# Kernel tuning notes

Hardware: AMD Instinct MI355X
Metric: run time of the kernel (lower is better)

## Reference

```python
import jax, jax.numpy as jnp
import numpy as np

NUM_GROUPS = 32
EPS = 1e-5


def group_norm(x, w, b):
    # x: [B, C, H, W]
    B, C, H, W = x.shape
    g = x.reshape(B, NUM_GROUPS, C // NUM_GROUPS, H, W)
    mu = g.mean(axis=(2, 3, 4), keepdims=True)
    var = g.var(axis=(2, 3, 4), keepdims=True)
    g = (g - mu) * jax.lax.rsqrt(var + EPS)
    x = g.reshape(B, C, H, W)
    return x * w[None, :, None, None] + b[None, :, None, None]


def conv1x1(x, w, b):
    # 1x1 conv == channel matmul; x: [B, C, H, W], w: [O, C], b: [O]
    return jnp.einsum('bchw,oc->bohw', x, w) + b[None, :, None, None]


def setup_inputs() -> dict:
    key = jax.random.key(0)
    ks = jax.random.split(key, 11)
    C = 512
    B, H, W = 4, 64, 64
    s = 1.0 / np.sqrt(C)
    return {
        'x': jax.random.normal(ks[0], (B, C, H, W), jnp.float32),
        'gn_w': jax.random.uniform(ks[1], (C,), jnp.float32, 0.5, 1.5),
        'gn_b': jax.random.normal(ks[2], (C,), jnp.float32) * 0.1,
        'wq': jax.random.normal(ks[3], (C, C), jnp.float32) * s,
        'bq': jax.random.normal(ks[4], (C,), jnp.float32) * 0.01,
        'wk': jax.random.normal(ks[5], (C, C), jnp.float32) * s,
        'bk': jax.random.normal(ks[6], (C,), jnp.float32) * 0.01,
        'wv': jax.random.normal(ks[7], (C, C), jnp.float32) * s,
        'bv': jax.random.normal(ks[8], (C,), jnp.float32) * 0.01,
        'wo': jax.random.normal(ks[9], (C, C), jnp.float32) * s,
        'bo': jax.random.normal(ks[10], (C,), jnp.float32) * 0.01,
    }


def reference(x, gn_w, gn_b, wq, bq, wk, bk, wv, bv, wo, bo):
    B, C, H, W = x.shape
    h_ = group_norm(x, gn_w, gn_b)
    q = conv1x1(h_, wq, bq).reshape(B, C, H * W)   # [B, C, HW]
    k = conv1x1(h_, wk, bk).reshape(B, C, H * W)
    v = conv1x1(h_, wv, bv).reshape(B, C, H * W)
    # scores: q^T k, scaled by C^-0.5; softmax over keys
    scores = jnp.einsum('bci,bcj->bij', q, k) * (C ** -0.5)  # [B, HW, HW]
    attn = jax.nn.softmax(scores, axis=-1)
    # h_[b,c,i] = sum_j v[b,c,j] * attn[b,i,j]
    h_ = jnp.einsum('bcj,bij->bci', v, attn).reshape(B, C, H, W)
    return x + conv1x1(h_, wo, bo)
```

## Files before the change

### kernel.cpp

```cpp
#include <hip/hip_runtime.h>
#include <hip/hip_bf16.h>

typedef __attribute__((ext_vector_type(8))) __bf16 bf16x8;
typedef __attribute__((ext_vector_type(4))) float f32x4;

__device__ __forceinline__ unsigned short f2bf(float f) {
  union { float f; unsigned u; } v; v.f = f;
  unsigned r = v.u + 0x7fffu + ((v.u >> 16) & 1u);
  return (unsigned short)(r >> 16);
}

__device__ __forceinline__ void gload_lds16(const void* g, void* s) {
  __builtin_amdgcn_global_load_lds(
      (const __attribute__((address_space(1))) void*)g,
      (__attribute__((address_space(3))) void*)s, 16, 0, 0);
}

__global__ __launch_bounds__(256) void convert_w(
    const float* __restrict__ wq, const float* __restrict__ wk,
    const float* __restrict__ wv, const float* __restrict__ wo,
    unsigned short* __restrict__ dst) {
  const int m = blockIdx.x >> 10;
  const float* src = (m == 0) ? wq : (m == 1) ? wk : (m == 2) ? wv : wo;
  const int idx = ((blockIdx.x & 1023) << 8) | threadIdx.x;
  dst[m * 262144 + idx] = f2bf(src[idx]);
}

__global__ __launch_bounds__(256) void zero_k(float* __restrict__ p, int n) {
  const int i = blockIdx.x * 256 + threadIdx.x;
  if (i < n) p[i] = 0.f;
}

__global__ __launch_bounds__(256) void gn_stats(
    const float* __restrict__ x, float2* __restrict__ partials) {
  const int bg = blockIdx.x >> 2, part = blockIdx.x & 3;
  const float* xg = x + (size_t)bg * 65536 + part * 1024;
  const int t = threadIdx.x;
  float s = 0.f, ss = 0.f;
#pragma unroll
  for (int r = 0; r < 16; ++r) {
    const float4 v = *(const float4*)(xg + (size_t)r * 4096 + t * 4);
    s += v.x + v.y + v.z + v.w;
    ss += v.x * v.x + v.y * v.y + v.z * v.z + v.w * v.w;
  }
#pragma unroll
  for (int m = 32; m; m >>= 1) { s += __shfl_xor(s, m); ss += __shfl_xor(ss, m); }
  __shared__ float red[8];
  const int wave = t >> 6, lane = t & 63;
  if (lane == 0) { red[wave] = s; red[wave + 4] = ss; }
  __syncthreads();
  if (t == 0) {
    float2 p;
    p.x = red[0] + red[1] + red[2] + red[3];
    p.y = red[4] + red[5] + red[6] + red[7];
    partials[blockIdx.x] = p;
  }
}

__global__ __launch_bounds__(256) void gn_apply(
    const float* __restrict__ x, const float2* __restrict__ partials,
    const float* __restrict__ gw, const float* __restrict__ gb,
    unsigned short* __restrict__ h_t) {
  const int bg = blockIdx.x >> 3, cc = blockIdx.x & 7;
  const int b = bg >> 5, g = bg & 31;
  const int t = threadIdx.x;
  __shared__ float chs[32];
  __shared__ unsigned short tile[16][520];
  if (t < 16) {
    const float2 p0 = partials[bg * 4 + 0], p1 = partials[bg * 4 + 1];
    const float2 p2 = partials[bg * 4 + 2], p3 = partials[bg * 4 + 3];
    const float S = p0.x + p1.x + p2.x + p3.x;
    const float SS = p0.y + p1.y + p2.y + p3.y;
    const float mu = S * (1.f / 65536.f);
    const float rstd = rsqrtf(SS * (1.f / 65536.f) - mu * mu + 1e-5f);
    const float sc = gw[g * 16 + t] * rstd;
    chs[t] = sc;
    chs[16 + t] = gb[g * 16 + t] - mu * sc;
  }
  __syncthreads();
  const float* xg = x + (size_t)bg * 65536 + cc * 512;
#pragma unroll
  for (int rr = 0; rr < 8; ++rr) {
    const int r = rr * 2 + (t >> 7), i = (t & 127) * 4;
    const float4 v = *(const float4*)(xg + (size_t)r * 4096 + i);
    const float sc = chs[r], sh = chs[16 + r];
    ushort4 o;
    o.x = f2bf(v.x * sc + sh); o.y = f2bf(v.y * sc + sh);
    o.z = f2bf(v.z * sc + sh); o.w = f2bf(v.w * sc + sh);
    *(ushort4*)&tile[r][i] = o;
  }
  __syncthreads();
  unsigned short* outp = h_t + ((size_t)b * 4096 + cc * 512) * 512 + g * 16;
#pragma unroll
  for (int rep = 0; rep < 4; ++rep) {
    const int task = rep * 256 + t;
    const int nl = task >> 1, half = (task & 1) * 8;
    ushort4 o0, o1;
    o0.x = tile[half + 0][nl]; o0.y = tile[half + 1][nl];
    o0.z = tile[half + 2][nl]; o0.w = tile[half + 3][nl];
    o1.x = tile[half + 4][nl]; o1.y = tile[half + 5][nl];
    o1.z = tile[half + 6][nl]; o1.w = tile[half + 7][nl];
    *(ushort4*)(outp + (size_t)nl * 512 + half) = o0;
    *(ushort4*)(outp + (size_t)nl * 512 + half + 4) = o1;
  }
}

__global__ __launch_bounds__(256) void reduce4_k(
    const float* __restrict__ part, const float* __restrict__ l,
    unsigned short* __restrict__ dst) {
  const size_t i = ((size_t)blockIdx.x * 256 + threadIdx.x) * 4;
  f32x4 s0 = *(const f32x4*)(part + i);
  f32x4 s1 = *(const f32x4*)(part + 2097152 + i);
  f32x4 s2 = *(const f32x4*)(part + 4194304 + i);
  f32x4 s3 = *(const f32x4*)(part + 6291456 + i);
  f32x4 s = (s0 + s1) + (s2 + s3);
  const float inv = 1.f / l[i >> 9];
  ushort4 o;
  o.x = f2bf(s[0] * inv); o.y = f2bf(s[1] * inv);
  o.z = f2bf(s[2] * inv); o.w = f2bf(s[3] * inv);
  *(ushort4*)(dst + i) = o;
}

__global__ __launch_bounds__(512, 4) void gemm_s256(
    const unsigned short* __restrict__ A, const unsigned short* __restrict__ Bt,
    unsigned short* __restrict__ Out, float* __restrict__ lsum) {
  __shared__ __align__(16) char smem[73728];
  const int tid = threadIdx.x;
  const int wave = tid >> 6, lane = tid & 63;
  const int l15 = lane & 15, l4 = lane >> 4;
  const int wm = wave >> 1, wn = wave & 1;

  const int bz = blockIdx.z;
  A += (size_t)bz * 2097152;
  Bt += (size_t)bz * 2097152;
  Out += (size_t)bz * 16777216;
  lsum += (size_t)bz * 4096;

  const int id = blockIdx.y * 32 + blockIdx.x;
  const int xcd = id & 7, j = id >> 3;
  const int by = ((xcd >> 1) << 2) + (j >> 4);
  const int bx = ((xcd & 1) << 4) + (j & 15);
  const int row0 = by << 8, col0 = bx << 7;

  const int ar = tid >> 2;
  const int akc = (tid & 3) ^ ((tid >> 4) & 3);

  auto stage = [&](int kt, int bi) {
    const int kb = kt << 5;
    char* base = smem + bi * 24576;
    const unsigned short* gA = A + (size_t)(row0 + ar) * 512 + kb + akc * 8;
    const unsigned short* gB = Bt + (size_t)(col0 + ar) * 512 + kb + akc * 8;
    gload_lds16(gA, base + wave * 1024);
    gload_lds16(gA + (size_t)128 * 512, base + 8192 + wave * 1024);
    gload_lds16(gB, base + 16384 + wave * 1024);
  };

  f32x4 acc[4][4];
#pragma unroll
  for (int r = 0; r < 4; ++r)
#pragma unroll
    for (int c = 0; c < 4; ++c) acc[r][c] = (f32x4)0.f;

  const int xsw = (l4 ^ (l15 >> 2)) << 4;

  auto compute = [&](int bi) {
    const char* pa = smem + bi * 24576 + (wm * 64 + l15) * 64 + xsw;
    const char* pb = smem + bi * 24576 + 16384 + (wn * 64 + l15) * 64 + xsw;
    bf16x8 af[4], bfr[4];
#pragma unroll
    for (int r = 0; r < 4; ++r) af[r] = *(const bf16x8*)(pa + r * 1024);
#pragma unroll
    for (int c = 0; c < 4; ++c) bfr[c] = *(const bf16x8*)(pb + c * 1024);
#pragma unroll
    for (int r = 0; r < 4; ++r)
#pragma unroll
      for (int c = 0; c < 4; ++c)
        acc[r][c] = __builtin_amdgcn_mfma_f32_16x16x32_bf16(af[r], bfr[c], acc[r][c], 0, 0, 0);
  };

  stage(0, 0);
  stage(1, 1);
  int bi = 0;
  for (int kt = 0; kt < 15; ++kt) {
    asm volatile("s_waitcnt vmcnt(3)" ::: "memory");
    __builtin_amdgcn_s_barrier();
    __builtin_amdgcn_sched_barrier(0);
    if (kt + 2 < 16) stage(kt + 2, (kt + 2) % 3);
    compute(bi);
    bi = (bi == 2) ? 0 : bi + 1;
  }
  asm volatile("s_waitcnt vmcnt(0)" ::: "memory");
  __builtin_amdgcn_s_barrier();
  __builtin_amdgcn_sched_barrier(0);
  compute(bi);

  __syncthreads();
  unsigned short* tile = (unsigned short*)smem;
#pragma unroll
  for (int p = 0; p < 2; ++p) {
    if ((wm >> 1) == p) {
#pragma unroll
      for (int c = 0; c < 4; ++c) {
        const int coll = wn * 64 + c * 16 + l15;
#pragma unroll
        for (int r = 0; r < 4; ++r) {
          const int rowl = (wm & 1) * 64 + r * 16 + l4 * 4;
#pragma unroll
          for (int j = 0; j < 4; ++j)
            tile[(rowl + j) * 136 + coll] = f2bf(__expf(acc[r][c][j]));
        }
      }
    }
    __syncthreads();
#pragma unroll
    for (int it = 0; it < 4; ++it) {
      const int idx = it * 512 + tid;
      const int rw = idx >> 4, ch = (idx & 15) * 8;
      const uint4 vv = *(const uint4*)&tile[rw * 136 + ch];
      *(uint4*)(Out + (size_t)(row0 + p * 128 + rw) * 4096 + col0 + ch) = vv;
      const unsigned* uu = (const unsigned*)&vv;
      float s = 0.f;
#pragma unroll
      for (int q = 0; q < 4; ++q) {
        union { unsigned u; float f; } w;
        w.u = uu[q] << 16; s += w.f;
        w.u = uu[q] & 0xffff0000u; s += w.f;
      }
      s += __shfl_xor(s, 1); s += __shfl_xor(s, 2);
      s += __shfl_xor(s, 4); s += __shfl_xor(s, 8);
      if ((lane & 15) == 0) atomicAdd(&lsum[row0 + p * 128 + rw], s);
    }
    __syncthreads();
  }
}

__global__ __launch_bounds__(512, 2) void gemm_s_ps(
    const unsigned short* __restrict__ A, const unsigned short* __restrict__ Bt,
    unsigned short* __restrict__ Out, float* __restrict__ lsum) {
  __shared__ __align__(16) char smem[147456];
  const int tid = threadIdx.x;
  const int wave = tid >> 6, lane = tid & 63;
  const int l15 = lane & 15, l4 = lane >> 4;
  const int wm = wave >> 1, wn = wave & 1;

  const int bz = blockIdx.z;
  A += (size_t)bz * 2097152;
  Bt += (size_t)bz * 2097152;
  Out += (size_t)bz * 16777216;
  lsum += (size_t)bz * 4096;

  const int id = blockIdx.y * 32 + blockIdx.x;
  const int xcd = id & 7, j = id >> 3;
  const int by = ((xcd >> 1) << 2) + (j >> 4);
  const int bx = ((xcd & 1) << 4) + (j & 15);
  const int row0 = by << 8, col0 = bx << 7;

  const int sr = tid >> 3;
  const int sc8 = (tid & 7) ^ (sr & 7);
  const unsigned short* gA = A + (size_t)(row0 + sr) * 512 + sc8 * 8;
  const unsigned short* gB = Bt + (size_t)(col0 + sr) * 512 + sc8 * 8;

  auto stA = [&](int kt, int bi, int p) {
    gload_lds16(gA + (size_t)(p << 6) * 512 + (kt << 6),
                smem + bi * 49152 + p * 8192 + wave * 1024);
  };
  auto stB = [&](int kt, int bi, int p) {
    gload_lds16(gB + (size_t)(p << 6) * 512 + (kt << 6),
                smem + bi * 49152 + 32768 + p * 8192 + wave * 1024);
  };

  f32x4 acc[4][4];
#pragma unroll
  for (int r = 0; r < 4; ++r)
#pragma unroll
    for (int c = 0; c < 4; ++c) acc[r][c] = (f32x4)0.f;

  const int sw0 = (l4 ^ (l15 & 7)) << 4;
  const int sw1 = ((4 + l4) ^ (l15 & 7)) << 4;
  const int arow = (wm * 64 + l15) << 7;
  const int brow = (wn * 64 + l15) << 7;

  bf16x8 bfr[4][2];

  stA(0, 0, 0); stA(0, 0, 1); stA(0, 0, 2); stA(0, 0, 3);
  stB(0, 0, 0); stB(0, 0, 1);
  stA(1, 1, 0); stA(1, 1, 1); stA(1, 1, 2); stA(1, 1, 3);
  stB(1, 1, 0); stB(1, 1, 1);
  asm volatile("s_waitcnt vmcnt(6)" ::: "memory");
  __builtin_amdgcn_s_barrier();
  __builtin_amdgcn_sched_barrier(0);

  int bi = 0;
#pragma unroll 1
  for (int kt = 0; kt < 8; ++kt) {
    const char* bufA = smem + bi * 49152;
    const char* bufB = bufA + 32768;
    const int pb = (bi + 2) % 3;
    const bool pre = (kt + 2 < 8);
    bf16x8 a0, a1;
    a0 = *(const bf16x8*)(bufA + arow + sw0);
    a1 = *(const bf16x8*)(bufA + arow + sw1);
#pragma unroll
    for (int c = 0; c < 4; ++c) {
      bfr[c][0] = *(const bf16x8*)(bufB + brow + c * 2048 + sw0);
      bfr[c][1] = *(const bf16x8*)(bufB + brow + c * 2048 + sw1);
    }
    if (pre) { stA(kt + 2, pb, 0); stA(kt + 2, pb, 1); }
    __builtin_amdgcn_s_barrier();
    asm volatile("s_waitcnt lgkmcnt(0)" ::: "memory");
    __builtin_amdgcn_sched_barrier(0);
    __builtin_amdgcn_s_setprio(1);
#pragma unroll
    for (int c = 0; c < 4; ++c) {
      acc[0][c] = __builtin_amdgcn_mfma_f32_16x16x32_bf16(a0, bfr[c][0], acc[0][c], 0, 0, 0);
      acc[0][c] = __builtin_amdgcn_mfma_f32_16x16x32_bf16(a1, bfr[c][1], acc[0][c], 0, 0, 0);
    }
    __builtin_amdgcn_s_setprio(0);
    __builtin_amdgcn_s_barrier();
    a0 = *(const bf16x8*)(bufA + arow + 2048 + sw0);
    a1 = *(const bf16x8*)(bufA + arow + 2048 + sw1);
    if (pre) { stA(kt + 2, pb, 2); stA(kt + 2, pb, 3); }
    __builtin_amdgcn_s_barrier();
    asm volatile("s_waitcnt lgkmcnt(0)" ::: "memory");
    __builtin_amdgcn_sched_barrier(0);
    __builtin_amdgcn_s_setprio(1);
#pragma unroll
    for (int c = 0; c < 4; ++c) {
      acc[1][c] = __builtin_amdgcn_mfma_f32_16x16x32_bf16(a0, bfr[c][0], acc[1][c], 0, 0, 0);
      acc[1][c] = __builtin_amdgcn_mfma_f32_16x16x32_bf16(a1, bfr[c][1], acc[1][c], 0, 0, 0);
    }
    __builtin_amdgcn_s_setprio(0);
    __builtin_amdgcn_s_barrier();
    a0 = *(const bf16x8*)(bufA + arow + 4096 + sw0);
    a1 = *(const bf16x8*)(bufA + arow + 4096 + sw1);
    if (pre) { stB(kt + 2, pb, 0); stB(kt + 2, pb, 1); }
    __builtin_amdgcn_s_barrier();
    asm volatile("s_waitcnt lgkmcnt(0)" ::: "memory");
    __builtin_amdgcn_sched_barrier(0);
    __builtin_amdgcn_s_setprio(1);
#pragma unroll
    for (int c = 0; c < 4; ++c) {
      acc[2][c] = __builtin_amdgcn_mfma_f32_16x16x32_bf16(a0, bfr[c][0], acc[2][c], 0, 0, 0);
      acc[2][c] = __builtin_amdgcn_mfma_f32_16x16x32_bf16(a1, bfr[c][1], acc[2][c], 0, 0, 0);
    }
    __builtin_amdgcn_s_setprio(0);
    __builtin_amdgcn_s_barrier();
    a0 = *(const bf16x8*)(bufA + arow + 6144 + sw0);
    a1 = *(const bf16x8*)(bufA + arow + 6144 + sw1);
    __builtin_amdgcn_s_barrier();
    asm volatile("s_waitcnt lgkmcnt(0)" ::: "memory");
    __builtin_amdgcn_sched_barrier(0);
    __builtin_amdgcn_s_setprio(1);
#pragma unroll
    for (int c = 0; c < 4; ++c) {
      acc[3][c] = __builtin_amdgcn_mfma_f32_16x16x32_bf16(a0, bfr[c][0], acc[3][c], 0, 0, 0);
      acc[3][c] = __builtin_amdgcn_mfma_f32_16x16x32_bf16(a1, bfr[c][1], acc[3][c], 0, 0, 0);
    }
    __builtin_amdgcn_s_setprio(0);
    if (pre) asm volatile("s_waitcnt vmcnt(6)" ::: "memory");
    else     asm volatile("s_waitcnt vmcnt(0)" ::: "memory");
    __builtin_amdgcn_s_barrier();
    __builtin_amdgcn_sched_barrier(0);
    bi = (bi == 2) ? 0 : bi + 1;
  }

  __syncthreads();
  unsigned short* tile = (unsigned short*)smem;
#pragma unroll
  for (int c = 0; c < 4; ++c) {
    const int coll = wn * 64 + c * 16 + l15;
#pragma unroll
    for (int r = 0; r < 4; ++r) {
      const int rowl = wm * 64 + r * 16 + l4 * 4;
#pragma unroll
      for (int j = 0; j < 4; ++j)
        tile[(rowl + j) * 136 + coll] = f2bf(__expf(acc[r][c][j]));
    }
  }
  __syncthreads();
#pragma unroll
  for (int it = 0; it < 8; ++it) {
    const int idx = it * 512 + tid;
    const int rw = idx >> 4, ch = (idx & 15) * 8;
    const uint4 vv = *(const uint4*)&tile[rw * 136 + ch];
    *(uint4*)(Out + (size_t)(row0 + rw) * 4096 + col0 + ch) = vv;
    const unsigned* uu = (const unsigned*)&vv;
    float s = 0.f;
#pragma unroll
    for (int q = 0; q < 4; ++q) {
      union { unsigned u; float f; } w;
      w.u = uu[q] << 16; s += w.f;
      w.u = uu[q] & 0xffff0000u; s += w.f;
    }
    s += __shfl_xor(s, 1); s += __shfl_xor(s, 2);
    s += __shfl_xor(s, 4); s += __shfl_xor(s, 8);
    if ((lane & 15) == 0) atomicAdd(&lsum[row0 + rw], s);
  }
}

__global__ __launch_bounds__(512, 2) void gemm_pv(
    const unsigned short* __restrict__ P, const unsigned short* __restrict__ Vt,
    unsigned short* __restrict__ Out, const float* __restrict__ lrow) {
  __shared__ __align__(16) char smem[147456];
  const int tid = threadIdx.x;
  const int wave = tid >> 6, lane = tid & 63;
  const int l15 = lane & 15, l4 = lane >> 4;
  const int wm = wave >> 1, wn = wave & 1;

  const int L = blockIdx.x + ((blockIdx.y + (blockIdx.z << 4)) << 2);
  const int xcd = L & 7, j = L >> 3;
  const int panel = xcd * 8 + (j >> 2);
  const int bx = j & 3, by = panel & 15, bz = panel >> 4;
  const int row0 = by << 8, col0 = bx << 7;
  P += (size_t)bz * 16777216;
  Vt += (size_t)bz * 2097152;
  Out += (size_t)bz * 2097152;
  lrow += bz * 4096;

  const int sr = tid >> 3;
  const int sc8 = (tid & 7) ^ (sr & 7);
  const unsigned short* gA = P + (size_t)(row0 + sr) * 4096 + sc8 * 8;
  const unsigned short* gB = Vt + (size_t)(col0 + sr) * 4096 + sc8 * 8;

  auto stA = [&](int kt, int bi, int p) {
    gload_lds16(gA + (size_t)(p << 6) * 4096 + (kt << 6),
                smem + bi * 49152 + p * 8192 + wave * 1024);
  };
  auto stB = [&](int kt, int bi, int p) {
    gload_lds16(gB + (size_t)(p << 6) * 4096 + (kt << 6),
                smem + bi * 49152 + 32768 + p * 8192 + wave * 1024);
  };

  f32x4 acc[4][4];
#pragma unroll
  for (int r = 0; r < 4; ++r)
#pragma unroll
    for (int c = 0; c < 4; ++c) acc[r][c] = (f32x4)0.f;

  const int sw0 = (l4 ^ (l15 & 7)) << 4;
  const int sw1 = ((4 + l4) ^ (l15 & 7)) << 4;
  const int arow = (wm * 64 + l15) << 7;
  const int brow = (wn * 64 + l15) << 7;

  bf16x8 bfr[4][2];

  stA(0, 0, 0); stA(0, 0, 1); stA(0, 0, 2); stA(0, 0, 3);
  stB(0, 0, 0); stB(0, 0, 1);
  stA(1, 1, 0); stA(1, 1, 1); stA(1, 1, 2); stA(1, 1, 3);
  stB(1, 1, 0); stB(1, 1, 1);
  asm volatile("s_waitcnt vmcnt(6)" ::: "memory");
  __builtin_amdgcn_s_barrier();
  __builtin_amdgcn_sched_barrier(0);

  int bi = 0;
#pragma unroll 1
  for (int kt = 0; kt < 64; ++kt) {
    const char* bufA = smem + bi * 49152;
    const char* bufB = bufA + 32768;
    const int pb = (bi + 2) % 3;
    const bool pre = (kt + 2 < 64);
    bf16x8 a0, a1;
    a0 = *(const bf16x8*)(bufA + arow + sw0);
    a1 = *(const bf16x8*)(bufA + arow + sw1);
#pragma unroll
    for (int c = 0; c < 4; ++c) {
      bfr[c][0] = *(const bf16x8*)(bufB + brow + c * 2048 + sw0);
      bfr[c][1] = *(const bf16x8*)(bufB + brow + c * 2048 + sw1);
    }
    if (pre) { stA(kt + 2, pb, 0); stA(kt + 2, pb, 1); }
    __builtin_amdgcn_s_barrier();
    asm volatile("s_waitcnt lgkmcnt(0)" ::: "memory");
    __builtin_amdgcn_sched_barrier(0);
    __builtin_amdgcn_s_setprio(1);
#pragma unroll
    for (int c = 0; c < 4; ++c) {
      acc[0][c] = __builtin_amdgcn_mfma_f32_16x16x32_bf16(a0, bfr[c][0], acc[0][c], 0, 0, 0);
      acc[0][c] = __builtin_amdgcn_mfma_f32_16x16x32_bf16(a1, bfr[c][1], acc[0][c], 0, 0, 0);
    }
    __builtin_amdgcn_s_setprio(0);
    __builtin_amdgcn_s_barrier();
    a0 = *(const bf16x8*)(bufA + arow + 2048 + sw0);
    a1 = *(const bf16x8*)(bufA + arow + 2048 + sw1);
    if (pre) { stA(kt + 2, pb, 2); stA(kt + 2, pb, 3); }
    __builtin_amdgcn_s_barrier();
    asm volatile("s_waitcnt lgkmcnt(0)" ::: "memory");
    __builtin_amdgcn_sched_barrier(0);
    __builtin_amdgcn_s_setprio(1);
#pragma unroll
    for (int c = 0; c < 4; ++c) {
      acc[1][c] = __builtin_amdgcn_mfma_f32_16x16x32_bf16(a0, bfr[c][0], acc[1][c], 0, 0, 0);
      acc[1][c] = __builtin_amdgcn_mfma_f32_16x16x32_bf16(a1, bfr[c][1], acc[1][c], 0, 0, 0);
    }
    __builtin_amdgcn_s_setprio(0);
    __builtin_amdgcn_s_barrier();
    a0 = *(const bf16x8*)(bufA + arow + 4096 + sw0);
    a1 = *(const bf16x8*)(bufA + arow + 4096 + sw1);
    if (pre) { stB(kt + 2, pb, 0); stB(kt + 2, pb, 1); }
    __builtin_amdgcn_s_barrier();
    asm volatile("s_waitcnt lgkmcnt(0)" ::: "memory");
    __builtin_amdgcn_sched_barrier(0);
    __builtin_amdgcn_s_setprio(1);
#pragma unroll
    for (int c = 0; c < 4; ++c) {
      acc[2][c] = __builtin_amdgcn_mfma_f32_16x16x32_bf16(a0, bfr[c][0], acc[2][c], 0, 0, 0);
      acc[2][c] = __builtin_amdgcn_mfma_f32_16x16x32_bf16(a1, bfr[c][1], acc[2][c], 0, 0, 0);
    }
    __builtin_amdgcn_s_setprio(0);
    __builtin_amdgcn_s_barrier();
    a0 = *(const bf16x8*)(bufA + arow + 6144 + sw0);
    a1 = *(const bf16x8*)(bufA + arow + 6144 + sw1);
    __builtin_amdgcn_s_barrier();
    asm volatile("s_waitcnt lgkmcnt(0)" ::: "memory");
    __builtin_amdgcn_sched_barrier(0);
    __builtin_amdgcn_s_setprio(1);
#pragma unroll
    for (int c = 0; c < 4; ++c) {
      acc[3][c] = __builtin_amdgcn_mfma_f32_16x16x32_bf16(a0, bfr[c][0], acc[3][c], 0, 0, 0);
      acc[3][c] = __builtin_amdgcn_mfma_f32_16x16x32_bf16(a1, bfr[c][1], acc[3][c], 0, 0, 0);
    }
    __builtin_amdgcn_s_setprio(0);
    if (pre) asm volatile("s_waitcnt vmcnt(6)" ::: "memory");
    else     asm volatile("s_waitcnt vmcnt(0)" ::: "memory");
    __builtin_amdgcn_s_barrier();
    __builtin_amdgcn_sched_barrier(0);
    bi = (bi == 2) ? 0 : bi + 1;
  }

  __syncthreads();
  unsigned short* tile = (unsigned short*)smem;
#pragma unroll
  for (int c = 0; c < 4; ++c) {
    const int coll = wn * 64 + c * 16 + l15;
#pragma unroll
    for (int r = 0; r < 4; ++r) {
      const int rowl = wm * 64 + r * 16 + l4 * 4;
#pragma unroll
      for (int j = 0; j < 4; ++j) {
        const float v = acc[r][c][j] * (1.0f / lrow[row0 + rowl + j]);
        tile[(rowl + j) * 136 + coll] = f2bf(v);
      }
    }
  }
  __syncthreads();
#pragma unroll
  for (int it = 0; it < 8; ++it) {
    const int idx = it * 512 + tid;
    const int rw = idx >> 4, ch = (idx & 15) * 8;
    const uint4 vv = *(const uint4*)&tile[rw * 136 + ch];
    *(uint4*)(Out + (size_t)(row0 + rw) * 512 + col0 + ch) = vv;
  }
}

template <bool OUT_BF16, int BIAS_MODE, bool RESID, bool TRANS_OUT, int SWZ,
          bool COAL>
__global__ __launch_bounds__(256) void gemm_bt(
    const unsigned short* __restrict__ A, long long sA, int lda,
    const unsigned short* __restrict__ Bt, long long sB, int ldb,
    void* __restrict__ OutV, long long sO, int ldo,
    const float* __restrict__ bias,
    const float* __restrict__ resid, long long sR,
    int K, float scale) {
  __shared__ __align__(16) char smem[49152];
  const int tid = threadIdx.x;
  const int wave = tid >> 6, lane = tid & 63;
  const int l15 = lane & 15, l4 = lane >> 4;
  const int wm = wave >> 1, wn = wave & 1;

  int bx = blockIdx.x, by = blockIdx.y, bz = blockIdx.z;
  if constexpr (SWZ == 1) {
    const int id = by * 32 + bx;
    const int xcd = id & 7, j = id >> 3;
    by = ((xcd >> 1) << 3) + (j >> 4);
    bx = ((xcd & 1) << 4) + (j & 15);
  } else if constexpr (SWZ == 2) {
    const int L = bx + ((by + (bz << 5)) << 2);
    const int xcd = L & 7, j = L >> 3;
    const int pair = xcd * 16 + (j >> 2);
    bx = j & 3;
    by = pair & 31;
    bz = pair >> 5;
  }
  const int row0 = by << 7, col0 = bx << 7;
  A += (size_t)bz * sA;
  Bt += (size_t)bz * sB;
  if (RESID) resid += (size_t)bz * sR;
  if constexpr (BIAS_MODE == 3) bias += (size_t)bz * sR;
  char* outB = (char*)OutV + (size_t)bz * sO * (OUT_BF16 ? 2 : 4);

  const int ar = tid >> 2;
  const int akc = (tid & 3) ^ ((tid >> 4) & 3);

  auto stage = [&](int kt, int bi) {
    const int kb = kt << 5;
    char* sAl = smem + bi * 16384 + wave * 1024;
    char* sBl = sAl + 8192;
    const unsigned short* gA = A + (size_t)(row0 + ar) * lda + kb + akc * 8;
    const unsigned short* gB = Bt + (size_t)(col0 + ar) * ldb + kb + akc * 8;
    gload_lds16(gA, sAl);
    gload_lds16(gB, sBl);
    gload_lds16(gA + (size_t)64 * lda, sAl + 4096);
    gload_lds16(gB + (size_t)64 * ldb, sBl + 4096);
  };

  f32x4 acc[4][4];
#pragma unroll
  for (int r = 0; r < 4; ++r)
#pragma unroll
    for (int c = 0; c < 4; ++c) acc[r][c] = (f32x4)0.f;

  const int nk = K >> 5;
  const int xsw = (l4 ^ (l15 >> 2)) << 4;

  auto compute = [&](int bi) {
    const char* pa = smem + bi * 16384 + (wm * 64 + l15) * 64 + xsw;
    const char* pb = smem + bi * 16384 + 8192 + (wn * 64 + l15) * 64 + xsw;
    bf16x8 af[4], bfr[4];
#pragma unroll
    for (int r = 0; r < 4; ++r) af[r] = *(const bf16x8*)(pa + r * 1024);
#pragma unroll
    for (int c = 0; c < 4; ++c) bfr[c] = *(const bf16x8*)(pb + c * 1024);
#pragma unroll
    for (int r = 0; r < 4; ++r)
#pragma unroll
      for (int c = 0; c < 4; ++c)
        acc[r][c] = __builtin_amdgcn_mfma_f32_16x16x32_bf16(af[r], bfr[c], acc[r][c], 0, 0, 0);
  };

  stage(0, 0);
  stage(1, 1);
  int bi = 0;
  for (int kt = 0; kt < nk - 1; ++kt) {
    asm volatile("s_waitcnt vmcnt(4)" ::: "memory");
    __builtin_amdgcn_s_barrier();
    __builtin_amdgcn_sched_barrier(0);
    if (kt + 2 < nk) stage(kt + 2, (kt + 2) % 3);
    compute(bi);
    bi = (bi == 2) ? 0 : bi + 1;
  }
  asm volatile("s_waitcnt vmcnt(0)" ::: "memory");
  __builtin_amdgcn_s_barrier();
  __builtin_amdgcn_sched_barrier(0);
  compute(bi);

  if constexpr (COAL && !TRANS_OUT) {
    __syncthreads();
    if constexpr (OUT_BF16) {
      unsigned short* tile = (unsigned short*)smem;
#pragma unroll
      for (int c = 0; c < 4; ++c) {
        const int coll = wn * 64 + c * 16 + l15;
        float badd = 0.f;
        if constexpr (BIAS_MODE == 1) badd = bias[col0 + coll];
#pragma unroll
        for (int r = 0; r < 4; ++r) {
          const int rowl = wm * 64 + r * 16 + l4 * 4;
#pragma unroll
          for (int j = 0; j < 4; ++j) {
            float v;
            if constexpr (BIAS_MODE == 3)
              v = acc[r][c][j] * (1.0f / bias[row0 + rowl + j]);
            else
              v = (acc[r][c][j] + badd) * scale;
            tile[(rowl + j) * 136 + coll] = f2bf(v);
          }
        }
      }
      __syncthreads();
      unsigned short* outp = (unsigned short*)outB;
#pragma unroll
      for (int it = 0; it < 8; ++it) {
        const int idx = it * 256 + tid;
        const int rw = idx >> 4, ch = (idx & 15) * 8;
        const uint4 vv = *(const uint4*)&tile[rw * 136 + ch];
        *(uint4*)(outp + (size_t)(row0 + rw) * ldo + col0 + ch) = vv;
      }
    } else {
      float* tile = (float*)smem;
#pragma unroll
      for (int p = 0; p < 2; ++p) {
        if (wm == p) {
#pragma unroll
          for (int c = 0; c < 4; ++c) {
            const int coll = wn * 64 + c * 16 + l15;
            float badd = 0.f;
            if constexpr (BIAS_MODE == 1) badd = bias[col0 + coll];
#pragma unroll
            for (int r = 0; r < 4; ++r) {
              const int rowl = r * 16 + l4 * 4;
#pragma unroll
              for (int j = 0; j < 4; ++j) {
                float v = acc[r][c][j] + badd;
                if constexpr (BIAS_MODE == 2) v += bias[row0 + p * 64 + rowl + j];
                tile[(rowl + j) * 132 + coll] = v * scale;
              }
            }
          }
        }
        __syncthreads();
        float* outp = (float*)outB;
#pragma unroll
        for (int it = 0; it < 8; ++it) {
          const int idx = it * 256 + tid;
          const int rw = idx >> 5, ch = (idx & 31) * 4;
          const int rowg = row0 + p * 64 + rw;
          f32x4 v = *(const f32x4*)&tile[rw * 132 + ch];
          if constexpr (RESID) {
            const float* rp = resid + (size_t)rowg * ldo + col0 + ch;
            v[0] += rp[0]; v[1] += rp[1]; v[2] += rp[2]; v[3] += rp[3];
          }
          *(f32x4*)(outp + (size_t)rowg * ldo + col0 + ch) = v;
        }
        __syncthreads();
      }
    }
  } else if constexpr (!TRANS_OUT) {
#pragma unroll
    for (int c = 0; c < 4; ++c) {
      const int colg = col0 + wn * 64 + c * 16 + l15;
      float badd = 0.f;
      if constexpr (BIAS_MODE == 1) badd = bias[colg];
#pragma unroll
      for (int r = 0; r < 4; ++r) {
        const int rowg = row0 + wm * 64 + r * 16 + l4 * 4;
#pragma unroll
        for (int j = 0; j < 4; ++j) {
          float v = acc[r][c][j] + badd;
          if constexpr (BIAS_MODE == 2) v += bias[rowg + j];
          v *= scale;
          if constexpr (RESID) v += resid[(size_t)(rowg + j) * ldo + colg];
          if constexpr (OUT_BF16)
            ((unsigned short*)outB)[(size_t)(rowg + j) * ldo + colg] = f2bf(v);
          else
            ((float*)outB)[(size_t)(rowg + j) * ldo + colg] = v;
        }
      }
    }
  } else {
    __syncthreads();
    unsigned short* tile = (unsigned short*)smem;
#pragma unroll
    for (int c = 0; c < 4; ++c) {
      const int coll = wn * 64 + c * 16 + l15;
      float badd = 0.f;
      if constexpr (BIAS_MODE == 1) badd = bias[col0 + coll];
#pragma unroll
      for (int r = 0; r < 4; ++r) {
        const int rowl = wm * 64 + r * 16 + l4 * 4;
#pragma unroll
        for (int j = 0; j < 4; ++j)
          tile[(rowl + j) * 132 + coll] = f2bf((acc[r][c][j] + badd) * scale);
      }
    }
    __syncthreads();
    unsigned short* outp = (unsigned short*)outB;
#pragma unroll 8
    for (int it = 0; it < 64; ++it) {
      const int idx = it * 256 + tid;
      const int cl = idx >> 7, il = idx & 127;
      outp[(size_t)(col0 + cl) * ldo + row0 + il] = tile[il * 132 + cl];
    }
  }
}

extern "C" void kernel_launch(void* const* d_in, const int* in_sizes, int n_in,
                              void* d_out, int out_size, void* d_ws, size_t ws_size,
                              hipStream_t stream) {
  const float* x   = (const float*)d_in[0];
  const float* gnw = (const float*)d_in[1];
  const float* gnb = (const float*)d_in[2];
  const float* wq  = (const float*)d_in[3];
  const float* bq  = (const float*)d_in[4];
  const float* wk  = (const float*)d_in[5];
  const float* bk  = (const float*)d_in[6];
  const float* wv  = (const float*)d_in[7];
  const float* bv  = (const float*)d_in[8];
  const float* wo  = (const float*)d_in[9];
  const float* bo  = (const float*)d_in[10];
  float* out = (float*)d_out;
  char* ws = (char*)d_ws;

  const size_t MB = 1u << 20;
  float2*         gnp  = (float2*)ws;
  float*          lrow = (float*)(ws + 64 * 1024);
  unsigned short* wbf  = (unsigned short*)(ws + 1 * MB);
  unsigned short* h_t  = (unsigned short*)(ws + 3 * MB);
  unsigned short* q_t  = (unsigned short*)(ws + 19 * MB);
  unsigned short* k_t  = (unsigned short*)(ws + 35 * MB);
  unsigned short* v_ct = (unsigned short*)(ws + 51 * MB);
  unsigned short* h2_t = (unsigned short*)(ws + 67 * MB);
  unsigned short* Pbuf = (unsigned short*)(ws + 83 * MB);
  float*          part = (float*)(ws + 115 * MB);

  const long long BS = 2097152;
  const long long PBS = 16777216;
  const float qscale = 0.044194173824159216f;
  const bool batched = ws_size >= 212 * MB;

  convert_w<<<dim3(4096), dim3(256), 0, stream>>>(wq, wk, wv, wo, wbf);
  gn_stats<<<dim3(512), dim3(256), 0, stream>>>(x, gnp);
  gn_apply<<<dim3(1024), dim3(256), 0, stream>>>(x, gnp, gnw, gnb, h_t);

  gemm_bt<true, 1, false, false, 0, true><<<dim3(4, 32, 4), 256, 0, stream>>>(
      h_t, BS, 512, wbf + 0, 0, 512, q_t, BS, 512, bq, nullptr, 0, 512, qscale);
  gemm_bt<true, 1, false, false, 0, true><<<dim3(4, 32, 4), 256, 0, stream>>>(
      h_t, BS, 512, wbf + 262144, 0, 512, k_t, BS, 512, bk, nullptr, 0, 512, 1.0f);
  gemm_bt<true, 1, false, true, 0, false><<<dim3(4, 32, 4), 256, 0, stream>>>(
      h_t, BS, 512, wbf + 524288, 0, 512, v_ct, BS, 4096, bv, nullptr, 0, 512, 1.0f);

  if (batched) {
    zero_k<<<dim3(64), dim3(256), 0, stream>>>(lrow, 16384);
    gemm_s_ps<<<dim3(32, 16, 4), dim3(512), 0, stream>>>(q_t, k_t, Pbuf, lrow);
    gemm_pv<<<dim3(4, 16, 4), dim3(512), 0, stream>>>(Pbuf, v_ct, h2_t, lrow);
  } else {
    for (int b = 0; b < 4; ++b) {
      zero_k<<<dim3(16), dim3(256), 0, stream>>>(lrow, 4096);
      gemm_s256<<<dim3(32, 16, 1), dim3(512), 0, stream>>>(
          q_t + (size_t)b * BS, k_t + (size_t)b * BS, Pbuf, lrow);
      gemm_bt<false, 0, false, false, 0, true><<<dim3(4, 32, 4), 256, 0, stream>>>(
          Pbuf, 1024, 4096, v_ct + (size_t)b * BS, 1024, 4096,
          part, 2097152, 512, nullptr, nullptr, 0, 1024, 1.0f);
      reduce4_k<<<dim3(2048), dim3(256), 0, stream>>>(part, lrow, h2_t + (size_t)b * BS);
    }
  }

  gemm_bt<false, 2, true, false, 0, true><<<dim3(32, 4, 4), 256, 0, stream>>>(
      wbf + 786432, 0, 512, h2_t, BS, 512, out, BS, 4096, bo, x, BS, 512, 1.0f);
}
```

Baseline: 295.9 us.

## Make score GEMM persistent, streaming row tiles through continuous K pipeline

Replaces the 2048-block score/exp kernel with a 256-block persistent kernel. Each block keeps one 128-column K tile and walks 8 row tiles of Q through a single 64-step triple-buffered pipeline. Prefetch of the next tile therefore overlaps the exp/bf16 store and row-sum epilogue of the previous tile. The epilogue now runs in two halves through a shared-memory buffer that is still in the prefetch rotation. This removes per-block launch and pipeline warm-up cost and improves K reuse, but adds risk around LDS buffer aliasing and serializes the epilogue inside the loop.

```diff
diff --git a/kernel.cpp b/kernel.cpp
--- a/kernel.cpp
+++ b/kernel.cpp
@@ -234,39 +234,39 @@
   }
 }
 
-__global__ __launch_bounds__(512, 2) void gemm_s_ps(
-    const unsigned short* __restrict__ A, const unsigned short* __restrict__ Bt,
-    unsigned short* __restrict__ Out, float* __restrict__ lsum) {
+__global__ __launch_bounds__(512, 2) void gemm_s_pers(
+    const unsigned short* __restrict__ Q, const unsigned short* __restrict__ Kt,
+    unsigned short* __restrict__ OutP, float* __restrict__ lsum) {
   __shared__ __align__(16) char smem[147456];
   const int tid = threadIdx.x;
   const int wave = tid >> 6, lane = tid & 63;
   const int l15 = lane & 15, l4 = lane >> 4;
   const int wm = wave >> 1, wn = wave & 1;
 
-  const int bz = blockIdx.z;
-  A += (size_t)bz * 2097152;
-  Bt += (size_t)bz * 2097152;
-  Out += (size_t)bz * 16777216;
-  lsum += (size_t)bz * 4096;
-
-  const int id = blockIdx.y * 32 + blockIdx.x;
-  const int xcd = id & 7, j = id >> 3;
-  const int by = ((xcd >> 1) << 2) + (j >> 4);
-  const int bx = ((xcd & 1) << 4) + (j & 15);
-  const int row0 = by << 8, col0 = bx << 7;
+  const int L = blockIdx.x;
+  const int xcd = L & 7, b32 = L >> 3;
+  const int bz = xcd >> 1;
+  const int col0 = ((xcd & 1) * 16 + (b32 & 15)) << 7;
+  const int byh = b32 >> 4;
+
+  const unsigned short* Qb = Q + (size_t)bz * 2097152;
+  const unsigned short* Kb = Kt + (size_t)bz * 2097152;
+  unsigned short* Ob = OutP + (size_t)bz * 16777216;
+  float* lb = lsum + bz * 4096;
 
   const int sr = tid >> 3;
   const int sc8 = (tid & 7) ^ (sr & 7);
-  const unsigned short* gA = A + (size_t)(row0 + sr) * 512 + sc8 * 8;
-  const unsigned short* gB = Bt + (size_t)(col0 + sr) * 512 + sc8 * 8;
-
-  auto stA = [&](int kt, int bi, int p) {
-    gload_lds16(gA + (size_t)(p << 6) * 512 + (kt << 6),
-                smem + bi * 49152 + p * 8192 + wave * 1024);
+  const unsigned short* gA0 = Qb + (size_t)sr * 512 + sc8 * 8;
+  const unsigned short* gB = Kb + (size_t)(col0 + sr) * 512 + sc8 * 8;
+
+  auto stA = [&](int s2, int p) {
+    const int r0 = (((s2 >> 3) * 2 + byh) << 8);
+    gload_lds16(gA0 + (size_t)(r0 + (p << 6)) * 512 + ((s2 & 7) << 6),
+                smem + (s2 % 3) * 49152 + p * 8192 + wave * 1024);
   };
-  auto stB = [&](int kt, int bi, int p) {
-    gload_lds16(gB + (size_t)(p << 6) * 512 + (kt << 6),
-                smem + bi * 49152 + 32768 + p * 8192 + wave * 1024);
+  auto stB = [&](int s2, int p) {
+    gload_lds16(gB + (size_t)(p << 6) * 512 + ((s2 & 7) << 6),
+                smem + (s2 % 3) * 49152 + 32768 + p * 8192 + wave * 1024);
   };
 
   f32x4 acc[4][4];
@@ -282,21 +282,18 @@
 
   bf16x8 bfr[4][2];
 
-  stA(0, 0, 0); stA(0, 0, 1); stA(0, 0, 2); stA(0, 0, 3);
-  stB(0, 0, 0); stB(0, 0, 1);
-  stA(1, 1, 0); stA(1, 1, 1); stA(1, 1, 2); stA(1, 1, 3);
-  stB(1, 1, 0); stB(1, 1, 1);
+  stA(0, 0); stA(0, 1); stA(0, 2); stA(0, 3); stB(0, 0); stB(0, 1);
+  stA(1, 0); stA(1, 1); stA(1, 2); stA(1, 3); stB(1, 0); stB(1, 1);
   asm volatile("s_waitcnt vmcnt(6)" ::: "memory");
   __builtin_amdgcn_s_barrier();
   __builtin_amdgcn_sched_barrier(0);
 
-  int bi = 0;
 #pragma unroll 1
-  for (int kt = 0; kt < 8; ++kt) {
-    const char* bufA = smem + bi * 49152;
+  for (int s = 0; s < 64; ++s) {
+    const char* bufA = smem + (s % 3) * 49152;
     const char* bufB = bufA + 32768;
-    const int pb = (bi + 2) % 3;
-    const bool pre = (kt + 2 < 8);
+    const int s2 = s + 2;
+    const bool pre = (s2 < 64);
     bf16x8 a0, a1;
     a0 = *(const bf16x8*)(bufA + arow + sw0);
     a1 = *(const bf16x8*)(bufA + arow + sw1);
@@ -305,7 +302,7 @@
       bfr[c][0] = *(const bf16x8*)(bufB + brow + c * 2048 + sw0);
       bfr[c][1] = *(const bf16x8*)(bufB + brow + c * 2048 + sw1);
     }
-    if (pre) { stA(kt + 2, pb, 0); stA(kt + 2, pb, 1); }
+    if (pre) { stA(s2, 0); stA(s2, 1); }
     __builtin_amdgcn_s_barrier();
     asm volatile("s_waitcnt lgkmcnt(0)" ::: "memory");
     __builtin_amdgcn_sched_barrier(0);
@@ -319,7 +316,7 @@
     __builtin_amdgcn_s_barrier();
     a0 = *(const bf16x8*)(bufA + arow + 2048 + sw0);
     a1 = *(const bf16x8*)(bufA + arow + 2048 + sw1);
-    if (pre) { stA(kt + 2, pb, 2); stA(kt + 2, pb, 3); }
+    if (pre) { stA(s2, 2); stA(s2, 3); }
     __builtin_amdgcn_s_barrier();
     asm volatile("s_waitcnt lgkmcnt(0)" ::: "memory");
     __builtin_amdgcn_sched_barrier(0);
@@ -333,7 +330,7 @@
     __builtin_amdgcn_s_barrier();
     a0 = *(const bf16x8*)(bufA + arow + 4096 + sw0);
     a1 = *(const bf16x8*)(bufA + arow + 4096 + sw1);
-    if (pre) { stB(kt + 2, pb, 0); stB(kt + 2, pb, 1); }
+    if (pre) { stB(s2, 0); stB(s2, 1); }
     __builtin_amdgcn_s_barrier();
     asm volatile("s_waitcnt lgkmcnt(0)" ::: "memory");
     __builtin_amdgcn_sched_barrier(0);
@@ -361,40 +358,53 @@
     else     asm volatile("s_waitcnt vmcnt(0)" ::: "memory");
     __builtin_amdgcn_s_barrier();
     __builtin_amdgcn_sched_barrier(0);
-    bi = (bi == 2) ? 0 : bi + 1;
-  }
-
-  __syncthreads();
-  unsigned short* tile = (unsigned short*)smem;
-#pragma unroll
-  for (int c = 0; c < 4; ++c) {
-    const int coll = wn * 64 + c * 16 + l15;
-#pragma unroll
-    for (int r = 0; r < 4; ++r) {
-      const int rowl = wm * 64 + r * 16 + l4 * 4;
-#pragma unroll
-      for (int j = 0; j < 4; ++j)
-        tile[(rowl + j) * 136 + coll] = f2bf(__expf(acc[r][c][j]));
-    }
-  }
-  __syncthreads();
-#pragma unroll
-  for (int it = 0; it < 8; ++it) {
-    const int idx = it * 512 + tid;
-    const int rw = idx >> 4, ch = (idx & 15) * 8;
-    const uint4 vv = *(const uint4*)&tile[rw * 136 + ch];
-    *(uint4*)(Out + (size_t)(row0 + rw) * 4096 + col0 + ch) = vv;
-    const unsigned* uu = (const unsigned*)&vv;
-    float s = 0.f;
-#pragma unroll
-    for (int q = 0; q < 4; ++q) {
-      union { unsigned u; float f; } w;
-      w.u = uu[q] << 16; s += w.f;
-      w.u = uu[q] & 0xffff0000u; s += w.f;
-    }
-    s += __shfl_xor(s, 1); s += __shfl_xor(s, 2);
-    s += __shfl_xor(s, 4); s += __shfl_xor(s, 8);
-    if ((lane & 15) == 0) atomicAdd(&lsum[row0 + rw], s);
+
+    if ((s & 7) == 7) {
+      const int row0 = (((s >> 3) * 2 + byh) << 8);
+      unsigned short* tile = (unsigned short*)(smem + (s % 3) * 49152);
+#pragma unroll
+      for (int p = 0; p < 2; ++p) {
+        if ((wm >> 1) == p) {
+#pragma unroll
+          for (int c = 0; c < 4; ++c) {
+            const int coll = wn * 64 + c * 16 + l15;
+#pragma unroll
+            for (int r = 0; r < 4; ++r) {
+              const int rowl = (wm & 1) * 64 + r * 16 + l4 * 4;
+#pragma unroll
+              for (int j = 0; j < 4; ++j)
+                tile[(rowl + j) * 136 + coll] = f2bf(__expf(acc[r][c][j]));
+            }
+          }
+        }
+        asm volatile("s_waitcnt lgkmcnt(0)" ::: "memory");
+        __builtin_amdgcn_s_barrier();
+#pragma unroll
+        for (int it = 0; it < 4; ++it) {
+          const int idx = it * 512 + tid;
+          const int rw = idx >> 4, ch = (idx & 15) * 8;
+          const uint4 vv = *(const uint4*)&tile[rw * 136 + ch];
+          *(uint4*)(Ob + (size_t)(row0 + p * 128 + rw) * 4096 + col0 + ch) = vv;
+          const unsigned* uu = (const unsigned*)&vv;
+          float rs = 0.f;
+#pragma unroll
+          for (int q = 0; q < 4; ++q) {
+            union { unsigned u; float f; } w;
+            w.u = uu[q] << 16; rs += w.f;
+            w.u = uu[q] & 0xffff0000u; rs += w.f;
+          }
+          rs += __shfl_xor(rs, 1); rs += __shfl_xor(rs, 2);
+          rs += __shfl_xor(rs, 4); rs += __shfl_xor(rs, 8);
+          if ((lane & 15) == 0) atomicAdd(&lb[row0 + p * 128 + rw], rs);
+        }
+        asm volatile("s_waitcnt lgkmcnt(0)" ::: "memory");
+        __builtin_amdgcn_s_barrier();
+      }
+#pragma unroll
+      for (int r = 0; r < 4; ++r)
+#pragma unroll
+        for (int c = 0; c < 4; ++c) acc[r][c] = (f32x4)0.f;
+    }
   }
 }
 
@@ -809,7 +819,7 @@
 
   if (batched) {
     zero_k<<<dim3(64), dim3(256), 0, stream>>>(lrow, 16384);
-    gemm_s_ps<<<dim3(32, 16, 4), dim3(512), 0, stream>>>(q_t, k_t, Pbuf, lrow);
+    gemm_s_pers<<<dim3(256), dim3(512), 0, stream>>>(q_t, k_t, Pbuf, lrow);
     gemm_pv<<<dim3(4, 16, 4), dim3(512), 0, stream>>>(Pbuf, v_ct, h2_t, lrow);
   } else {
     for (int b = 0; b < 4; ++b) {
```

Result: no change. 297.6 us (+0.6%).
